# Kernel optimization log

Measured on AMD Instinct MI355X. Metric: run time of the kernel, lower is better.

## Reference

```python
import jax, jax.numpy as jnp
import numpy as np

B, L, D_IN, D_OUT = 4, 2048, 4096, 4096


def setup_inputs() -> dict:
    key = jax.random.key(0)
    k1, k2, k3, k4 = jax.random.split(key, 4)
    x = jax.random.normal(k1, (B, L, D_IN), dtype=jnp.float32)
    # base weight stored transposed as [in, out], like self.base = base.T
    base = jax.random.normal(k2, (D_IN, D_OUT), dtype=jnp.float32) * 0.02
    # binary delta sign mask in {0, 1}, stored transposed [in, out]
    mask = jax.random.randint(k3, (D_IN, D_OUT), 0, 2).astype(jnp.int32)
    # coeff = mean(|finetune - base|); a small positive scalar
    coeff = jax.random.uniform(k4, (1,), dtype=jnp.float32) * 0.01
    return {"x": x, "base": base, "coeff": coeff, "mask": mask}


def reference(x, base, coeff, mask):
    # Original: x @ base.T_stored + coeff * (x @ repeated_mask)
    # (t_coeff * x) @ mask == t_coeff * (x @ mask); we avoid materializing the
    # per-batch repeated mask since broadcasting the [in, out] mask is equivalent.
    m = mask.astype(x.dtype)            # {0,1} dequantized mask, [in, out]
    c = coeff[0].astype(x.dtype)
    return jnp.einsum('bld,de->ble', x, base) + c * jnp.einsum('bld,de->ble', x, m)
```

## Files before the change

kernel.cpp:

```cpp
#include <hip/hip_runtime.h>
#include <hip/hip_bf16.h>
#include <stdint.h>

#define DIN 4096
#define DOUT 4096
#define NK 128

typedef __attribute__((ext_vector_type(8))) short short8;
typedef __attribute__((ext_vector_type(8))) unsigned short ushort8;
typedef __attribute__((ext_vector_type(16))) float f32x16;

__device__ inline unsigned short f2bf(float f) {
    union { float f; unsigned u; } v; v.f = f;
    unsigned r = v.u + 0x7fffu + ((v.u >> 16) & 1u);
    return (unsigned short)(r >> 16);
}


__global__ void cvt_x_blocked(const float* __restrict__ x, ushort* __restrict__ xb) {
    const int t = threadIdx.x;
    const int bx = blockIdx.x;
    const int R = bx >> 6, u = bx & 63;
    const int r32 = t >> 3, kcol = t & 7;
    const int kk = kcol >> 2, s = (kcol >> 1) & 1, h = kcol & 1;
    const float* src = x + ((size_t)R * 256) * DIN + u * 64 + kcol * 8;
    ushort* dst = xb + (size_t)R * 1048576 + (size_t)u * 16384
                + (size_t)kk * 8192 + s * 512 + h * 256 + r32 * 8;
#pragma unroll
    for (int j = 0; j < 8; ++j) {
        const float* p = src + ((size_t)(j * 32 + r32)) * DIN;
        float4 v0 = *(const float4*)p, v1 = *(const float4*)(p + 4);
        ushort8 o;
        o[0] = f2bf(v0.x); o[1] = f2bf(v0.y); o[2] = f2bf(v0.z); o[3] = f2bf(v0.w);
        o[4] = f2bf(v1.x); o[5] = f2bf(v1.y); o[6] = f2bf(v1.z); o[7] = f2bf(v1.w);
        *(ushort8*)(dst + (size_t)j * 1024) = o;
    }
}

__global__ void make_wt_kernel(const float* __restrict__ base, const int* __restrict__ mask,
                               const float* __restrict__ coeff, ushort* __restrict__ wt) {
    __shared__ float tile[64][65];
    const float c = coeff[0];
    const int t = threadIdx.x;
    const int bd = blockIdx.x >> 6;
    const int be = blockIdx.x & 63;
    const int d0 = bd * 64, e0 = be * 64;
#pragma unroll
    for (int i = 0; i < 4; ++i) {
        int idx = i * 256 + t;
        int r = idx >> 4;
        int c4 = (idx & 15) << 2;
        const float4 bv = *(const float4*)(base + (size_t)(d0 + r) * DOUT + e0 + c4);
        const int4  mv = *(const int4*)(mask + (size_t)(d0 + r) * DOUT + e0 + c4);
        tile[r][c4 + 0] = bv.x + c * (float)mv.x;
        tile[r][c4 + 1] = bv.y + c * (float)mv.y;
        tile[r][c4 + 2] = bv.z + c * (float)mv.z;
        tile[r][c4 + 3] = bv.w + c * (float)mv.w;
    }
    __syncthreads();
#pragma unroll
    for (int i = 0; i < 8; ++i) {
        int idx = i * 256 + t;
        int r = idx >> 5;
        int p = (idx & 31) << 1;
        ushort2 o;
        o.x = f2bf(tile[p][r]);
        o.y = f2bf(tile[p + 1][r]);
        *(ushort2*)(wt + (size_t)(e0 + r) * DIN + d0 + p) = o;
    }
}

__global__ void reblock_w(const ushort* __restrict__ wt_rm, ushort* __restrict__ wb) {
    const int t = threadIdx.x;
    const int bx = blockIdx.x;
    const int R = bx >> 6, u = bx & 63;
    const int r32 = t >> 3, kcol = t & 7;
    const int kk = kcol >> 2, s = (kcol >> 1) & 1, h = kcol & 1;
    const ushort* src = wt_rm + ((size_t)R * 256) * DIN + u * 64 + kcol * 8;
    ushort* dst = wb + (size_t)R * 1048576 + (size_t)u * 16384
                + (size_t)kk * 8192 + s * 512 + h * 256 + r32 * 8;
#pragma unroll
    for (int j = 0; j < 8; ++j) {
        ushort8 o = *(const ushort8*)(src + ((size_t)(j * 32 + r32)) * DIN);
        *(ushort8*)(dst + (size_t)j * 1024) = o;
    }
}


#define MFMA32(D, VA, VB) D = __builtin_amdgcn_mfma_f32_32x32x16_bf16(VA, VB, D, 0, 0, 0)

#define RB(P,N,S) (*(const short8*)&lB[P][bw + (N)*1024 + (S)*512])

#define STEP(P, AC, AN, BSW, BSL, AOFF, GW, GA, GL, LOFF) \
  { \
    short8 b00=RB(P,0,0),b01=RB(P,0,1),b10=RB(P,1,0),b11=RB(P,1,1); \
    short8 b20=RB(P,2,0),b21=RB(P,2,1),b30=RB(P,3,0),b31=RB(P,3,1); \
    if (GA) { AN##0=*(const short8*)(aP+(AOFF));      AN##1=*(const short8*)(aP+(AOFF)+512); \
              AN##2=*(const short8*)(aP+(AOFF)+1024); AN##3=*(const short8*)(aP+(AOFF)+1536); } \
    if (GW) { *(short8*)&lB[1-(P)][dw] = BSW##0; *(short8*)&lB[1-(P)][dw+4096] = BSW##1; } \
    if (GL) { BSL##0 = *(const short8*)(bP+(LOFF)); BSL##1 = *(const short8*)(bP+(LOFF)+4096); } \
    __builtin_amdgcn_s_setprio(1); \
    MFMA32(c00, AC##0, b00); MFMA32(c00, AC##1, b01); \
    MFMA32(c01, AC##0, b10); MFMA32(c01, AC##1, b11); \
    MFMA32(c02, AC##0, b20); MFMA32(c02, AC##1, b21); \
    MFMA32(c03, AC##0, b30); MFMA32(c03, AC##1, b31); \
    MFMA32(c10, AC##2, b00); MFMA32(c10, AC##3, b01); \
    MFMA32(c11, AC##2, b10); MFMA32(c11, AC##3, b11); \
    MFMA32(c12, AC##2, b20); MFMA32(c12, AC##3, b21); \
    MFMA32(c13, AC##2, b30); MFMA32(c13, AC##3, b31); \
    __builtin_amdgcn_s_setprio(0); \
    asm volatile("s_waitcnt lgkmcnt(0)" ::: "memory"); \
    __builtin_amdgcn_s_barrier(); \
    __builtin_amdgcn_sched_barrier(0); \
  }

__global__ __launch_bounds__(512, 2) void gemm_kernel(const ushort* __restrict__ A,
                                                      const ushort* __restrict__ Bt,
                                                      float* __restrict__ C) {
    __shared__ __align__(16) ushort lB[2][8192];

    const int tid = threadIdx.x;
    const int lane = tid & 63;
    const int wave = tid >> 6;

    const int nbn = DOUT / 256;
    const int nwg = gridDim.x;
    int bid = blockIdx.x;
    int cpx = nwg >> 3;
    int s = (bid & 7) * cpx + (bid >> 3);
    const int m0 = (s / nbn) * 256;
    const int n0 = (s % nbn) * 256;

    const int wr = wave >> 1;
    const int wc = wave & 1;
    const int fr = lane & 31;
    const int fq = lane >> 5;

    const int bw = wc * 4096 + fq * 256 + fr * 8;
    const int dw = tid * 8;

    const ushort* aP = A + (size_t)(m0 >> 8) * 1048576
                     + (wr * 2) * 1024 + fq * 256 + fr * 8;
    const ushort* bP = Bt + (size_t)(n0 >> 8) * 1048576 + tid * 8;

    f32x16 c00 = {}, c01 = {}, c02 = {}, c03 = {};
    f32x16 c10 = {}, c11 = {}, c12 = {}, c13 = {};
    short8 aE0, aE1, aE2, aE3, aO0, aO1, aO2, aO3;
    short8 bsE0, bsE1, bsO0, bsO1;

    {
        short8 t0 = *(const short8*)(bP);
        short8 t1 = *(const short8*)(bP + 4096);
        bsO0 = *(const short8*)(bP + 8192);
        bsO1 = *(const short8*)(bP + 8192 + 4096);
        aE0 = *(const short8*)(aP);        aE1 = *(const short8*)(aP + 512);
        aE2 = *(const short8*)(aP + 1024); aE3 = *(const short8*)(aP + 1536);
        *(short8*)&lB[0][dw] = t0;
        *(short8*)&lB[0][dw + 4096] = t1;
        asm volatile("s_waitcnt lgkmcnt(0)" ::: "memory");
        __builtin_amdgcn_s_barrier();
        __builtin_amdgcn_sched_barrier(0);
    }

    for (int v = 0; v < NK; v += 2) {
        const bool g = (v < NK - 2);
        STEP(0, aE, aO, bsO, bsE, 8192, 1, 1, g, 16384)
        STEP(1, aO, aE, bsE, bsO, 16384, g, g, g, 24576)
        aP += 16384; bP += 16384;
    }

    const int gcb = n0 + wc * 128 + fr;
    const int grb = m0 + wr * 64 + fq * 4;
#define WRT(CT, MT, NN) \
    _Pragma("unroll") \
    for (int r = 0; r < 16; ++r) { \
        int grow = grb + (MT) * 32 + (r & 3) + 8 * (r >> 2); \
        C[(size_t)grow * DOUT + gcb + (NN) * 32] = CT[r]; \
    }
    WRT(c00, 0, 0) WRT(c01, 0, 1) WRT(c02, 0, 2) WRT(c03, 0, 3)
    WRT(c10, 1, 0) WRT(c11, 1, 1) WRT(c12, 1, 2) WRT(c13, 1, 3)
#undef WRT
}

extern "C" void kernel_launch(void* const* d_in, const int* in_sizes, int n_in,
                              void* d_out, int out_size, void* d_ws, size_t ws_size,
                              hipStream_t stream) {
    const float* x = (const float*)d_in[0];
    const float* base = (const float*)d_in[1];
    const float* coeff = (const float*)d_in[2];
    const int* mask = (const int*)d_in[3];
    float* out = (float*)d_out;

    const int M = in_sizes[0] / DIN;
    ushort* xb = (ushort*)d_ws;
    ushort* wb = xb + (size_t)M * DIN;
    ushort* wt_rm = (ushort*)d_out;

    cvt_x_blocked<<<(M / 256) * 64, 256, 0, stream>>>(x, xb);
    make_wt_kernel<<<(DIN / 64) * (DOUT / 64), 256, 0, stream>>>(base, mask, coeff, wt_rm);
    reblock_w<<<(DOUT / 256) * 64, 256, 0, stream>>>(wt_rm, wb);

    const int nwg = (M / 256) * (DOUT / 256);
    gemm_kernel<<<nwg, 512, 0, stream>>>(xb, wb, out);
}
```

Before: 379.2 us.

## Load B fragments directly from global into registers, drop LDS staging

The GEMM no longer stages the B tile through double-buffered shared memory with per-step barriers. Each wave now loads its own B fragments straight from global memory into registers, double-buffered like A. This removes LDS writes, LDS reads and workgroup barriers. In exchange, global and L2 traffic for B grows because the two wave rows no longer share loads, and register pressure rises with 16 B fragment registers per wave.

```diff
diff --git a/kernel.cpp b/kernel.cpp
--- a/kernel.cpp
+++ b/kernel.cpp
@@ -89,36 +89,31 @@
 
 #define MFMA32(D, VA, VB) D = __builtin_amdgcn_mfma_f32_32x32x16_bf16(VA, VB, D, 0, 0, 0)
 
-#define RB(P,N,S) (*(const short8*)&lB[P][bw + (N)*1024 + (S)*512])
+#define PRIO1 __builtin_amdgcn_s_setprio(1);
+#define PRIO0 __builtin_amdgcn_s_setprio(0);
 
-#define STEP(P, AC, AN, BSW, BSL, AOFF, GW, GA, GL, LOFF) \
-  { \
-    short8 b00=RB(P,0,0),b01=RB(P,0,1),b10=RB(P,1,0),b11=RB(P,1,1); \
-    short8 b20=RB(P,2,0),b21=RB(P,2,1),b30=RB(P,3,0),b31=RB(P,3,1); \
-    if (GA) { AN##0=*(const short8*)(aP+(AOFF));      AN##1=*(const short8*)(aP+(AOFF)+512); \
-              AN##2=*(const short8*)(aP+(AOFF)+1024); AN##3=*(const short8*)(aP+(AOFF)+1536); } \
-    if (GW) { *(short8*)&lB[1-(P)][dw] = BSW##0; *(short8*)&lB[1-(P)][dw+4096] = BSW##1; } \
-    if (GL) { BSL##0 = *(const short8*)(bP+(LOFF)); BSL##1 = *(const short8*)(bP+(LOFF)+4096); } \
-    __builtin_amdgcn_s_setprio(1); \
-    MFMA32(c00, AC##0, b00); MFMA32(c00, AC##1, b01); \
-    MFMA32(c01, AC##0, b10); MFMA32(c01, AC##1, b11); \
-    MFMA32(c02, AC##0, b20); MFMA32(c02, AC##1, b21); \
-    MFMA32(c03, AC##0, b30); MFMA32(c03, AC##1, b31); \
-    MFMA32(c10, AC##2, b00); MFMA32(c10, AC##3, b01); \
-    MFMA32(c11, AC##2, b10); MFMA32(c11, AC##3, b11); \
-    MFMA32(c12, AC##2, b20); MFMA32(c12, AC##3, b21); \
-    MFMA32(c13, AC##2, b30); MFMA32(c13, AC##3, b31); \
-    __builtin_amdgcn_s_setprio(0); \
-    asm volatile("s_waitcnt lgkmcnt(0)" ::: "memory"); \
-    __builtin_amdgcn_s_barrier(); \
-    __builtin_amdgcn_sched_barrier(0); \
-  }
+#define LDA(X, OFF) { \
+    X##0 = *(const short8*)(aP + (OFF));        X##1 = *(const short8*)(aP + (OFF) + 512); \
+    X##2 = *(const short8*)(aP + (OFF) + 1024); X##3 = *(const short8*)(aP + (OFF) + 1536); }
+#define LDB(X, OFF) { \
+    X##0 = *(const short8*)(bP + (OFF));        X##1 = *(const short8*)(bP + (OFF) + 512); \
+    X##2 = *(const short8*)(bP + (OFF) + 1024); X##3 = *(const short8*)(bP + (OFF) + 1536); \
+    X##4 = *(const short8*)(bP + (OFF) + 2048); X##5 = *(const short8*)(bP + (OFF) + 2560); \
+    X##6 = *(const short8*)(bP + (OFF) + 3072); X##7 = *(const short8*)(bP + (OFF) + 3584); }
+
+#define MFMA16(AX, BX) \
+    MFMA32(c00, AX##0, BX##0); MFMA32(c00, AX##1, BX##1); \
+    MFMA32(c01, AX##0, BX##2); MFMA32(c01, AX##1, BX##3); \
+    MFMA32(c02, AX##0, BX##4); MFMA32(c02, AX##1, BX##5); \
+    MFMA32(c03, AX##0, BX##6); MFMA32(c03, AX##1, BX##7); \
+    MFMA32(c10, AX##2, BX##0); MFMA32(c10, AX##3, BX##1); \
+    MFMA32(c11, AX##2, BX##2); MFMA32(c11, AX##3, BX##3); \
+    MFMA32(c12, AX##2, BX##4); MFMA32(c12, AX##3, BX##5); \
+    MFMA32(c13, AX##2, BX##6); MFMA32(c13, AX##3, BX##7);
 
 __global__ __launch_bounds__(512, 2) void gemm_kernel(const ushort* __restrict__ A,
                                                       const ushort* __restrict__ Bt,
                                                       float* __restrict__ C) {
-    __shared__ __align__(16) ushort lB[2][8192];
-
     const int tid = threadIdx.x;
     const int lane = tid & 63;
     const int wave = tid >> 6;
@@ -136,38 +131,29 @@
     const int fr = lane & 31;
     const int fq = lane >> 5;
 
-    const int bw = wc * 4096 + fq * 256 + fr * 8;
-    const int dw = tid * 8;
-
-    const ushort* aP = A + (size_t)(m0 >> 8) * 1048576
+    const ushort* aP = A  + (size_t)(m0 >> 8) * 1048576
                      + (wr * 2) * 1024 + fq * 256 + fr * 8;
-    const ushort* bP = Bt + (size_t)(n0 >> 8) * 1048576 + tid * 8;
+    const ushort* bP = Bt + (size_t)(n0 >> 8) * 1048576
+                     + (wc * 4) * 1024 + fq * 256 + fr * 8;
 
     f32x16 c00 = {}, c01 = {}, c02 = {}, c03 = {};
     f32x16 c10 = {}, c11 = {}, c12 = {}, c13 = {};
     short8 aE0, aE1, aE2, aE3, aO0, aO1, aO2, aO3;
-    short8 bsE0, bsE1, bsO0, bsO1;
+    short8 bE0, bE1, bE2, bE3, bE4, bE5, bE6, bE7;
+    short8 bO0, bO1, bO2, bO3, bO4, bO5, bO6, bO7;
 
-    {
-        short8 t0 = *(const short8*)(bP);
-        short8 t1 = *(const short8*)(bP + 4096);
-        bsO0 = *(const short8*)(bP + 8192);
-        bsO1 = *(const short8*)(bP + 8192 + 4096);
-        aE0 = *(const short8*)(aP);        aE1 = *(const short8*)(aP + 512);
-        aE2 = *(const short8*)(aP + 1024); aE3 = *(const short8*)(aP + 1536);
-        *(short8*)&lB[0][dw] = t0;
-        *(short8*)&lB[0][dw + 4096] = t1;
-        asm volatile("s_waitcnt lgkmcnt(0)" ::: "memory");
-        __builtin_amdgcn_s_barrier();
-        __builtin_amdgcn_sched_barrier(0);
-    }
+    LDA(aE, 0) LDB(bE, 0)
 
-    for (int v = 0; v < NK; v += 2) {
-        const bool g = (v < NK - 2);
-        STEP(0, aE, aO, bsO, bsE, 8192, 1, 1, g, 16384)
-        STEP(1, aO, aE, bsE, bsO, 16384, g, g, g, 24576)
+    for (int v = 0; v < NK - 2; v += 2) {
+        LDA(aO, 8192)  LDB(bO, 8192)
+        PRIO1 MFMA16(aE, bE) PRIO0
+        LDA(aE, 16384) LDB(bE, 16384)
+        PRIO1 MFMA16(aO, bO) PRIO0
         aP += 16384; bP += 16384;
     }
+    LDA(aO, 8192) LDB(bO, 8192)
+    PRIO1 MFMA16(aE, bE) PRIO0
+    PRIO1 MFMA16(aO, bO) PRIO0
 
     const int gcb = n0 + wc * 128 + fr;
     const int grb = m0 + wr * 64 + fq * 4;
```

New measurement: 417.0 us. +9.9%, slower.
